# Performance work log

Measured on AMD Instinct MI355X. Metric: run time of the kernel, lower is better.

## Reference

```python
import jax, jax.numpy as jnp
import numpy as np
from jax import lax

K = 3          # kernel_size
PAD = 1        # replication padding
EPS = 1e-5     # BatchNorm2d eps


def setup_inputs() -> dict:
    key = jax.random.key(0)
    k1, k2, k3, k4 = jax.random.split(key, 4)
    B, Cin, O, H, W = 16, 64, 128, 32, 32
    x = jax.random.normal(k1, (B, Cin + 5, H, W), dtype=jnp.float32)
    conv_w = jax.random.normal(k2, (O, Cin, K, K), dtype=jnp.float32) * 0.05
    conv_b = jax.random.normal(k3, (O,), dtype=jnp.float32) * 0.05
    shapes_kernel = jax.random.normal(k4, (O, 5, K * K), dtype=jnp.float32)
    return {"x": x, "conv_w": conv_w, "conv_b": conv_b, "shapes_kernel": shapes_kernel}


def _bn_noaffine(y):
    # BatchNorm2d(affine=False) in training mode: batch stats over (N, H, W)
    m = jnp.mean(y, axis=(0, 2, 3), keepdims=True)
    v = jnp.mean((y - m) ** 2, axis=(0, 2, 3), keepdims=True)
    return (y - m) / jnp.sqrt(v + EPS)


def reference(x, conv_w, conv_b, shapes_kernel):
    B = x.shape[0]
    # replication padding
    xp = jnp.pad(x, ((0, 0), (0, 0), (PAD, PAD), (PAD, PAD)), mode="edge")
    feat, shp = xp[:, :-5], xp[:, -5:]

    # conv branch: VALID conv on feature channels -> (B, O, H, W)
    conv_out = lax.conv_general_dilated(
        feat, conv_w, window_strides=(1, 1), padding="VALID",
        dimension_numbers=("NCHW", "OIHW", "NCHW"),
    ) + conv_b[None, :, None, None]
    H, W = conv_out.shape[2], conv_out.shape[3]
    NW = H * W

    # unfold(x_padded[:, -5:], K): patches (B, 5, K*K, NW), channel-major like torch
    patches = jnp.stack(
        [shp[:, :, i:i + H, j:j + W] for i in range(K) for j in range(K)], axis=2
    ).reshape(B, 5, K * K, NW)

    # center the first two (x,y coordinate) channels on the window center
    c = K * K // 2
    centered_xy = patches[:, :2] - patches[:, :2, c:c + 1]
    windows = jnp.concatenate([centered_xy, patches[:, 2:]], axis=1)  # (B,5,KK,NW)

    # L1 distance against learned shape kernel: (B, O, NW)
    delta = windows[:, None] - shapes_kernel[None, :, :, :, None]  # (B,O,5,KK,NW)
    shape_difference = jnp.sum(jnp.abs(delta), axis=(2, 3))

    # fold with (1,1) kernel == reshape to image
    sdw = shape_difference.reshape(B, -1, H, W)
    muxed = jax.nn.relu(_bn_noaffine(sdw))

    conv_bn = _bn_noaffine(conv_out)
    attended = jax.nn.relu(conv_bn - muxed)

    # pass the 5 shape channels through unchanged
    return jnp.concatenate([attended, x[:, -5:]], axis=1)
```

## Files before the change

kernel.cpp:

```cpp
#include <hip/hip_runtime.h>

typedef __attribute__((ext_vector_type(8))) __bf16 bf16x8;
typedef __attribute__((ext_vector_type(4))) float f32x4;

#define NB 16
#define CIN 64
#define CT 69
#define NO 128
#define HWSZ 1024
#define OUTC 133

__device__ __forceinline__ unsigned pack_bf16(float a, float b) {
    unsigned ua = __float_as_uint(a);
    ua += 0x7fffu + ((ua >> 16) & 1u);
    unsigned ub = __float_as_uint(b);
    ub += 0x7fffu + ((ub >> 16) & 1u);
    return (ua >> 16) | (ub & 0xffff0000u);
}

__device__ __forceinline__ void gload16(const void* g, void* l) {
    __builtin_amdgcn_global_load_lds(
        (const __attribute__((address_space(1))) unsigned int*)g,
        (__attribute__((address_space(3))) unsigned int*)l, 16, 0, 0);
}

__global__ __launch_bounds__(512) void prep_sdw_kernel(
    const float* __restrict__ x, const float* __restrict__ cw,
    const float* __restrict__ sk, unsigned* __restrict__ xT,
    unsigned* __restrict__ wT, float* __restrict__ sdw,
    float* __restrict__ sdwpart, float* __restrict__ out)
{
    int bl = blockIdx.x;
    int tid = threadIdx.x;

    if (bl < 512) {
        int chg = bl >> 5;
        int slice = bl & 31;
        int pix = slice * 512 + tid;
        int b = pix >> 10;
        int hw = pix & 1023;
        int h = hw >> 5, w = hw & 31;

        float win[45];
#pragma unroll
        for (int ch = 0; ch < 5; ++ch) {
            const float* xb = x + (((size_t)b * CT + CIN + ch) << 10);
#pragma unroll
            for (int ki = 0; ki < 3; ++ki) {
                int rr = h + ki - 1;
                rr = rr < 0 ? 0 : (rr > 31 ? 31 : rr);
                const float* rp = xb + (rr << 5);
#pragma unroll
                for (int kj = 0; kj < 3; ++kj) {
                    int cc = w + kj - 1;
                    cc = cc < 0 ? 0 : (cc > 31 ? 31 : cc);
                    win[ch * 9 + ki * 3 + kj] = rp[cc];
                }
            }
        }
#pragma unroll
        for (int ch = 0; ch < 2; ++ch) {
            float c = win[ch * 9 + 4];
#pragma unroll
            for (int k = 0; k < 9; ++k) win[ch * 9 + k] -= c;
        }
#pragma unroll
        for (int q = 0; q < 45; ++q) asm volatile("" : "+v"(win[q]));

        int wid = tid >> 6;
        int wslot = slice * 8 + wid;
        for (int j = 0; j < 8; ++j) {
            int ch = chg * 8 + j;
            const float* kk = sk + (size_t)ch * 45;
            float s = 0.f;
#pragma unroll
            for (int q = 0; q < 45; ++q) s += fabsf(win[q] - kk[q]);
            sdw[(((size_t)b * NO + ch) << 10) + hw] = s;
            float ps = s, ps2 = s * s;
#pragma unroll
            for (int off = 32; off; off >>= 1) {
                ps  += __shfl_xor(ps, off);
                ps2 += __shfl_xor(ps2, off);
            }
            if ((tid & 63) == 0) {
                sdwpart[((size_t)ch * 256 + wslot) * 2]     = ps;
                sdwpart[((size_t)ch * 256 + wslot) * 2 + 1] = ps2;
            }
        }
    } else if (bl < 768) {
        int v = (bl - 512) * 512 + tid;
        int blk2 = v >> 8;
        int t2 = v & 255;
        int b = blk2 >> 5, h = blk2 & 31;
        int w = t2 & 31, cp0 = t2 >> 5;
        const float* xr = x + (((size_t)b * CT) << 10) + h * 32 + w;
        unsigned* dst = xT + (size_t)blk2 * 1024 + w * 32;
        int sw = (w & 7) << 2;
#pragma unroll
        for (int r = 0; r < 4; ++r) {
            int cp = cp0 + r * 8;
            dst[cp ^ sw] = pack_bf16(xr[(size_t)(2 * cp) << 10],
                                     xr[(size_t)(2 * cp + 1) << 10]);
        }
    } else if (bl < 776) {
        int tg = (bl - 768) * 512 + tid;
        int o = tg >> 5, cp = tg & 31;
        int sw = (o & 7) << 2;
#pragma unroll
        for (int tap = 0; tap < 9; ++tap) {
            float v0 = cw[((size_t)o * CIN + 2 * cp) * 9 + tap];
            float v1 = cw[((size_t)o * CIN + 2 * cp + 1) * 9 + tap];
            wT[tap * 4096 + o * 32 + (cp ^ sw)] = pack_bf16(v0, v1);
        }
    } else {
        int idx = (bl - 776) * 512 + tid;
        int q = idx & 255;
        int c = (idx >> 8) % 5;
        int b = (idx >> 8) / 5;
        ((float4*)out)[((size_t)b * OUTC + NO + c) * 256 + q] =
            ((const float4*)x)[((size_t)b * CT + CIN + c) * 256 + q];
    }
}

__global__ __launch_bounds__(512) void conv_mfma_kernel(
    const char* __restrict__ xT, const char* __restrict__ wT,
    float* __restrict__ out, float* __restrict__ convpart)
{
    __shared__ __align__(16) char smem[49152];
    char* Xs = smem;
    char* W0 = smem + 16384;
    char* W1 = smem + 32768;

    int bid = blockIdx.x;
    int b = bid >> 4;
    int h0 = (bid & 15) * 2;

    int tid = threadIdx.x;
    int lane = tid & 63;
    int wid = tid >> 6;
    int lo = lane & 15, g = lane >> 4;
    int ks = wid >> 2;
    int mg = (wid >> 1) & 1;
    int ng = wid & 1;

#pragma unroll
    for (int q = 0; q < 2; ++q) {
        int ch = wid * 2 + q;
        int s = ch >> 2;
        int srch = h0 - 1 + s; srch = srch < 0 ? 0 : (srch > 31 ? 31 : srch);
        gload16(xT + ((size_t)(b * 32 + srch)) * 4096 + (ch & 3) * 1024 + lane * 16,
                Xs + ch * 1024);
    }
#pragma unroll
    for (int q = 0; q < 2; ++q) {
        int ch = wid * 2 + q;
        gload16(wT + ch * 1024 + lane * 16, W0 + ch * 1024);
    }

    int acol[2][3];
#pragma unroll
    for (int i = 0; i < 2; ++i)
#pragma unroll
        for (int kj = 0; kj < 3; ++kj) {
            int cin = i * 16 + lo + kj - 1;
            cin = cin < 0 ? 0 : (cin > 31 ? 31 : cin);
            acol[i][kj] = cin * 128 + ((ks * 64 + g * 16) ^ ((cin & 7) << 4));
        }
    int boff[4];
#pragma unroll
    for (int n = 0; n < 4; ++n) {
        int o = ng * 64 + n * 16 + lo;
        boff[n] = o * 128 + ((ks * 64 + g * 16) ^ ((o & 7) << 4));
    }

    f32x4 acc[2][4];
#pragma unroll
    for (int i = 0; i < 2; ++i)
#pragma unroll
        for (int n = 0; n < 4; ++n) acc[i][n] = (f32x4){0.f, 0.f, 0.f, 0.f};

    __syncthreads();

#pragma unroll
    for (int tap = 0; tap < 9; ++tap) {
        int ki = tap / 3, kj = tap % 3;
        if (tap < 8) {
            char* wn = ((tap + 1) & 1) ? W1 : W0;
#pragma unroll
            for (int q = 0; q < 2; ++q) {
                int ch = wid * 2 + q;
                gload16(wT + (size_t)(tap + 1) * 16384 + ch * 1024 + lane * 16,
                        wn + ch * 1024);
            }
        }
        const char* wc = (tap & 1) ? W1 : W0;
        bf16x8 a0 = *(const bf16x8*)(Xs + (mg + ki) * 4096 + acol[0][kj]);
        bf16x8 a1 = *(const bf16x8*)(Xs + (mg + ki) * 4096 + acol[1][kj]);
#pragma unroll
        for (int n = 0; n < 4; ++n) {
            bf16x8 bv = *(const bf16x8*)(wc + boff[n]);
            acc[0][n] = __builtin_amdgcn_mfma_f32_16x16x32_bf16(a0, bv, acc[0][n], 0, 0, 0);
            acc[1][n] = __builtin_amdgcn_mfma_f32_16x16x32_bf16(a1, bv, acc[1][n], 0, 0, 0);
        }
        __syncthreads();
    }

    float* T = (float*)smem;
    if (ks == 1) {
#pragma unroll
        for (int i = 0; i < 2; ++i)
#pragma unroll
            for (int n = 0; n < 4; ++n)
#pragma unroll
                for (int r = 0; r < 4; ++r) {
                    int pixel = (mg * 2 + i) * 16 + g * 4 + r;
                    int o = ng * 64 + n * 16 + lo;
                    T[pixel * 129 + o] = acc[i][n][r];
                }
    }
    __syncthreads();
    if (ks == 0) {
#pragma unroll
        for (int i = 0; i < 2; ++i)
#pragma unroll
            for (int n = 0; n < 4; ++n)
#pragma unroll
                for (int r = 0; r < 4; ++r) {
                    int pixel = (mg * 2 + i) * 16 + g * 4 + r;
                    int o = ng * 64 + n * 16 + lo;
                    T[pixel * 129 + o] += acc[i][n][r];
                }
    }
    __syncthreads();
    float* obase = out + (((size_t)b * OUTC) << 10) + h0 * 32;
#pragma unroll
    for (int r = 0; r < 4; ++r) {
        int o = r * 32 + (tid >> 4);
        int pq = tid & 15;
        float4 v;
        v.x = T[(pq * 4 + 0) * 129 + o];
        v.y = T[(pq * 4 + 1) * 129 + o];
        v.z = T[(pq * 4 + 2) * 129 + o];
        v.w = T[(pq * 4 + 3) * 129 + o];
        *(float4*)(obase + ((size_t)o << 10) + pq * 4) = v;
        float s  = v.x + v.y + v.z + v.w;
        float s2 = v.x * v.x + v.y * v.y + v.z * v.z + v.w * v.w;
#pragma unroll
        for (int off = 1; off < 16; off <<= 1) {
            s  += __shfl_xor(s, off);
            s2 += __shfl_xor(s2, off);
        }
        if (pq == 0) {
            convpart[((size_t)o * 256 + bid) * 2]     = s;
            convpart[((size_t)o * 256 + bid) * 2 + 1] = s2;
        }
    }
}

__global__ __launch_bounds__(512) void final_kernel(
    const float* __restrict__ sdw, const float* __restrict__ convpart,
    const float* __restrict__ sdwpart, float* __restrict__ out)
{
    __shared__ float st[32];
    int bl = blockIdx.x;
    int tid = threadIdx.x;
    int b = bl >> 4;
    int o0 = (bl & 15) * 8;

    int lane = tid & 63;
    int wid = tid >> 6;
    {
        int ch = o0 + wid;
        double cs = 0.0, cs2 = 0.0, ss = 0.0, ss2 = 0.0;
#pragma unroll
        for (int q = 0; q < 4; ++q) {
            int slot = lane + q * 64;
            const float* cp = convpart + ((size_t)ch * 256 + slot) * 2;
            cs  += cp[0]; cs2 += cp[1];
            const float* sp = sdwpart + ((size_t)ch * 256 + slot) * 2;
            ss  += sp[0]; ss2 += sp[1];
        }
#pragma unroll
        for (int off = 32; off; off >>= 1) {
            cs  += __shfl_down(cs, off);
            cs2 += __shfl_down(cs2, off);
            ss  += __shfl_down(ss, off);
            ss2 += __shfl_down(ss2, off);
        }
        if (lane == 0) {
            double n = 16384.0;
            double cm = cs / n, cv = cs2 / n - cm * cm;
            double sm = ss / n, sv = ss2 / n - sm * sm;
            st[wid * 4]     = (float)cm;
            st[wid * 4 + 1] = (float)(1.0 / sqrt(cv + 1e-5));
            st[wid * 4 + 2] = (float)sm;
            st[wid * 4 + 3] = (float)(1.0 / sqrt(sv + 1e-5));
        }
    }
    __syncthreads();

    float4* outq = (float4*)out;
    const float4* sdwq = (const float4*)sdw;
#pragma unroll
    for (int k = 0; k < 4; ++k) {
        int ql = tid + k * 512;
        int pl = ql >> 8;
        int q = ql & 255;
        int o = o0 + pl;
        float4 cvv = outq[((size_t)b * OUTC + o) * 256 + q];
        float4 svv = sdwq[((size_t)b * NO + o) * 256 + q];
        float cm = st[pl * 4], cis = st[pl * 4 + 1];
        float sm = st[pl * 4 + 2], sis = st[pl * 4 + 3];
        float4 rv;
        {
            float mu = (svv.x - sm) * sis; mu = mu > 0.f ? mu : 0.f;
            float v = (cvv.x - cm) * cis - mu; rv.x = v > 0.f ? v : 0.f;
        }
        {
            float mu = (svv.y - sm) * sis; mu = mu > 0.f ? mu : 0.f;
            float v = (cvv.y - cm) * cis - mu; rv.y = v > 0.f ? v : 0.f;
        }
        {
            float mu = (svv.z - sm) * sis; mu = mu > 0.f ? mu : 0.f;
            float v = (cvv.z - cm) * cis - mu; rv.z = v > 0.f ? v : 0.f;
        }
        {
            float mu = (svv.w - sm) * sis; mu = mu > 0.f ? mu : 0.f;
            float v = (cvv.w - cm) * cis - mu; rv.w = v > 0.f ? v : 0.f;
        }
        outq[((size_t)b * OUTC + o) * 256 + q] = rv;
    }
}

extern "C" void kernel_launch(void* const* d_in, const int* in_sizes, int n_in,
                              void* d_out, int out_size, void* d_ws, size_t ws_size,
                              hipStream_t stream)
{
    const float* x  = (const float*)d_in[0];
    const float* cw = (const float*)d_in[1];
    const float* sk = (const float*)d_in[3];
    float* out = (float*)d_out;

    float*    sdw      = (float*)d_ws;
    unsigned* xT       = (unsigned*)((char*)d_ws + 0x810000);
    unsigned* wT       = (unsigned*)((char*)d_ws + 0xA10000);
    float*    convpart = (float*)((char*)d_ws + 0xA40000);
    float*    sdwpart  = (float*)((char*)d_ws + 0xA80000);

    prep_sdw_kernel<<<816, 512, 0, stream>>>(x, cw, sk, xT, wT, sdw, sdwpart, out);
    conv_mfma_kernel<<<256, 512, 0, stream>>>((const char*)xT, (const char*)wT,
                                              out, convpart);
    final_kernel   <<<256, 512, 0, stream>>>(sdw, convpart, sdwpart, out);
}
```

Baseline: 36.37 us.

## Fuse conv and final BN kernels via cooperative grid sync; triple-buffer weight loads

Merges the conv MFMA kernel and the final BN/ReLU kernel into one cooperative launch, using a grid-wide sync after the per-block statistics are written. This removes one kernel launch and its gap. It also switches the per-tap weight staging from double to triple buffering, with explicit vmcnt waits and one barrier per tap. The cost is a larger LDS footprint and the overhead of a cooperative launch plus a grid barrier. All 256 blocks must also be co-resident.

```diff
diff --git a/kernel.cpp b/kernel.cpp
--- a/kernel.cpp
+++ b/kernel.cpp
@@ -1,4 +1,7 @@
 #include <hip/hip_runtime.h>
+#include <hip/hip_cooperative_groups.h>
+
+namespace cg = cooperative_groups;
 
 typedef __attribute__((ext_vector_type(8))) __bf16 bf16x8;
 typedef __attribute__((ext_vector_type(4))) float f32x4;
@@ -122,14 +125,18 @@
     }
 }
 
-__global__ __launch_bounds__(512) void conv_mfma_kernel(
+__global__ __launch_bounds__(512) void conv_final_kernel(
     const char* __restrict__ xT, const char* __restrict__ wT,
-    float* __restrict__ out, float* __restrict__ convpart)
+    const float* __restrict__ sdw, float* __restrict__ convpart,
+    const float* __restrict__ sdwpart, float* __restrict__ out)
 {
-    __shared__ __align__(16) char smem[49152];
+    __shared__ __align__(16) char smem[65536];
+    cg::grid_group gg = cg::this_grid();
+
     char* Xs = smem;
-    char* W0 = smem + 16384;
-    char* W1 = smem + 32768;
+    char* Wb0 = smem + 16384;
+    char* Wb1 = smem + 32768;
+    char* Wb2 = smem + 49152;
 
     int bid = blockIdx.x;
     int b = bid >> 4;
@@ -154,7 +161,12 @@
 #pragma unroll
     for (int q = 0; q < 2; ++q) {
         int ch = wid * 2 + q;
-        gload16(wT + ch * 1024 + lane * 16, W0 + ch * 1024);
+        gload16(wT + ch * 1024 + lane * 16, Wb0 + ch * 1024);
+    }
+#pragma unroll
+    for (int q = 0; q < 2; ++q) {
+        int ch = wid * 2 + q;
+        gload16(wT + 16384 + ch * 1024 + lane * 16, Wb1 + ch * 1024);
     }
 
     int acol[2][3];
@@ -179,21 +191,24 @@
 #pragma unroll
         for (int n = 0; n < 4; ++n) acc[i][n] = (f32x4){0.f, 0.f, 0.f, 0.f};
 
-    __syncthreads();
-
 #pragma unroll
     for (int tap = 0; tap < 9; ++tap) {
         int ki = tap / 3, kj = tap % 3;
-        if (tap < 8) {
-            char* wn = ((tap + 1) & 1) ? W1 : W0;
+        if (tap == 8) asm volatile("s_waitcnt vmcnt(0)" ::: "memory");
+        else          asm volatile("s_waitcnt vmcnt(2)" ::: "memory");
+        __builtin_amdgcn_sched_barrier(0);
+        __builtin_amdgcn_s_barrier();
+        __builtin_amdgcn_sched_barrier(0);
+        if (tap + 2 < 9) {
+            char* wn = ((tap + 2) % 3 == 0) ? Wb0 : ((tap + 2) % 3 == 1) ? Wb1 : Wb2;
 #pragma unroll
             for (int q = 0; q < 2; ++q) {
                 int ch = wid * 2 + q;
-                gload16(wT + (size_t)(tap + 1) * 16384 + ch * 1024 + lane * 16,
+                gload16(wT + (size_t)(tap + 2) * 16384 + ch * 1024 + lane * 16,
                         wn + ch * 1024);
             }
         }
-        const char* wc = (tap & 1) ? W1 : W0;
+        const char* wc = (tap % 3 == 0) ? Wb0 : (tap % 3 == 1) ? Wb1 : Wb2;
         bf16x8 a0 = *(const bf16x8*)(Xs + (mg + ki) * 4096 + acol[0][kj]);
         bf16x8 a1 = *(const bf16x8*)(Xs + (mg + ki) * 4096 + acol[1][kj]);
 #pragma unroll
@@ -202,8 +217,8 @@
             acc[0][n] = __builtin_amdgcn_mfma_f32_16x16x32_bf16(a0, bv, acc[0][n], 0, 0, 0);
             acc[1][n] = __builtin_amdgcn_mfma_f32_16x16x32_bf16(a1, bv, acc[1][n], 0, 0, 0);
         }
-        __syncthreads();
-    }
+    }
+    __syncthreads();
 
     float* T = (float*)smem;
     if (ks == 1) {
@@ -255,80 +270,74 @@
             convpart[((size_t)o * 256 + bid) * 2 + 1] = s2;
         }
     }
-}
-
-__global__ __launch_bounds__(512) void final_kernel(
-    const float* __restrict__ sdw, const float* __restrict__ convpart,
-    const float* __restrict__ sdwpart, float* __restrict__ out)
-{
-    __shared__ float st[32];
-    int bl = blockIdx.x;
-    int tid = threadIdx.x;
-    int b = bl >> 4;
-    int o0 = (bl & 15) * 8;
-
-    int lane = tid & 63;
-    int wid = tid >> 6;
+
+    __threadfence();
+    gg.sync();
+
     {
-        int ch = o0 + wid;
-        double cs = 0.0, cs2 = 0.0, ss = 0.0, ss2 = 0.0;
-#pragma unroll
-        for (int q = 0; q < 4; ++q) {
-            int slot = lane + q * 64;
-            const float* cp = convpart + ((size_t)ch * 256 + slot) * 2;
-            cs  += cp[0]; cs2 += cp[1];
-            const float* sp = sdwpart + ((size_t)ch * 256 + slot) * 2;
-            ss  += sp[0]; ss2 += sp[1];
-        }
-#pragma unroll
-        for (int off = 32; off; off >>= 1) {
-            cs  += __shfl_down(cs, off);
-            cs2 += __shfl_down(cs2, off);
-            ss  += __shfl_down(ss, off);
-            ss2 += __shfl_down(ss2, off);
-        }
-        if (lane == 0) {
-            double n = 16384.0;
-            double cm = cs / n, cv = cs2 / n - cm * cm;
-            double sm = ss / n, sv = ss2 / n - sm * sm;
-            st[wid * 4]     = (float)cm;
-            st[wid * 4 + 1] = (float)(1.0 / sqrt(cv + 1e-5));
-            st[wid * 4 + 2] = (float)sm;
-            st[wid * 4 + 3] = (float)(1.0 / sqrt(sv + 1e-5));
-        }
-    }
-    __syncthreads();
-
-    float4* outq = (float4*)out;
-    const float4* sdwq = (const float4*)sdw;
-#pragma unroll
-    for (int k = 0; k < 4; ++k) {
-        int ql = tid + k * 512;
-        int pl = ql >> 8;
-        int q = ql & 255;
-        int o = o0 + pl;
-        float4 cvv = outq[((size_t)b * OUTC + o) * 256 + q];
-        float4 svv = sdwq[((size_t)b * NO + o) * 256 + q];
-        float cm = st[pl * 4], cis = st[pl * 4 + 1];
-        float sm = st[pl * 4 + 2], sis = st[pl * 4 + 3];
-        float4 rv;
+        float* st = (float*)smem;
+        int o0 = (bid & 15) * 8;
         {
-            float mu = (svv.x - sm) * sis; mu = mu > 0.f ? mu : 0.f;
-            float v = (cvv.x - cm) * cis - mu; rv.x = v > 0.f ? v : 0.f;
-        }
-        {
-            float mu = (svv.y - sm) * sis; mu = mu > 0.f ? mu : 0.f;
-            float v = (cvv.y - cm) * cis - mu; rv.y = v > 0.f ? v : 0.f;
-        }
-        {
-            float mu = (svv.z - sm) * sis; mu = mu > 0.f ? mu : 0.f;
-            float v = (cvv.z - cm) * cis - mu; rv.z = v > 0.f ? v : 0.f;
-        }
-        {
-            float mu = (svv.w - sm) * sis; mu = mu > 0.f ? mu : 0.f;
-            float v = (cvv.w - cm) * cis - mu; rv.w = v > 0.f ? v : 0.f;
-        }
-        outq[((size_t)b * OUTC + o) * 256 + q] = rv;
+            int ch = o0 + wid;
+            double cs = 0.0, cs2 = 0.0, ss = 0.0, ss2 = 0.0;
+#pragma unroll
+            for (int q = 0; q < 4; ++q) {
+                int slot = lane + q * 64;
+                const float* cp = convpart + ((size_t)ch * 256 + slot) * 2;
+                cs  += cp[0]; cs2 += cp[1];
+                const float* sp = sdwpart + ((size_t)ch * 256 + slot) * 2;
+                ss  += sp[0]; ss2 += sp[1];
+            }
+#pragma unroll
+            for (int off = 32; off; off >>= 1) {
+                cs  += __shfl_down(cs, off);
+                cs2 += __shfl_down(cs2, off);
+                ss  += __shfl_down(ss, off);
+                ss2 += __shfl_down(ss2, off);
+            }
+            if (lane == 0) {
+                double n = 16384.0;
+                double cm = cs / n, cv = cs2 / n - cm * cm;
+                double sm = ss / n, sv = ss2 / n - sm * sm;
+                st[wid * 4]     = (float)cm;
+                st[wid * 4 + 1] = (float)(1.0 / sqrt(cv + 1e-5));
+                st[wid * 4 + 2] = (float)sm;
+                st[wid * 4 + 3] = (float)(1.0 / sqrt(sv + 1e-5));
+            }
+        }
+        __syncthreads();
+
+        float4* outq = (float4*)out;
+        const float4* sdwq = (const float4*)sdw;
+#pragma unroll
+        for (int k = 0; k < 4; ++k) {
+            int ql = tid + k * 512;
+            int pl = ql >> 8;
+            int q = ql & 255;
+            int o = o0 + pl;
+            float4 cvv = outq[((size_t)b * OUTC + o) * 256 + q];
+            float4 svv = sdwq[((size_t)b * NO + o) * 256 + q];
+            float cm = st[pl * 4], cis = st[pl * 4 + 1];
+            float sm = st[pl * 4 + 2], sis = st[pl * 4 + 3];
+            float4 rv;
+            {
+                float mu = (svv.x - sm) * sis; mu = mu > 0.f ? mu : 0.f;
+                float v = (cvv.x - cm) * cis - mu; rv.x = v > 0.f ? v : 0.f;
+            }
+            {
+                float mu = (svv.y - sm) * sis; mu = mu > 0.f ? mu : 0.f;
+                float v = (cvv.y - cm) * cis - mu; rv.y = v > 0.f ? v : 0.f;
+            }
+            {
+                float mu = (svv.z - sm) * sis; mu = mu > 0.f ? mu : 0.f;
+                float v = (cvv.z - cm) * cis - mu; rv.z = v > 0.f ? v : 0.f;
+            }
+            {
+                float mu = (svv.w - sm) * sis; mu = mu > 0.f ? mu : 0.f;
+                float v = (cvv.w - cm) * cis - mu; rv.w = v > 0.f ? v : 0.f;
+            }
+            outq[((size_t)b * OUTC + o) * 256 + q] = rv;
+        }
     }
 }
 
@@ -348,7 +357,13 @@
     float*    sdwpart  = (float*)((char*)d_ws + 0xA80000);
 
     prep_sdw_kernel<<<816, 512, 0, stream>>>(x, cw, sk, xT, wT, sdw, sdwpart, out);
-    conv_mfma_kernel<<<256, 512, 0, stream>>>((const char*)xT, (const char*)wT,
-                                              out, convpart);
-    final_kernel   <<<256, 512, 0, stream>>>(sdw, convpart, sdwpart, out);
-}
+
+    const char* xTc = (const char*)xT;
+    const char* wTc = (const char*)wT;
+    const float* sdwc = sdw;
+    const float* sdwpartc = sdwpart;
+    void* args[] = {(void*)&xTc, (void*)&wTc, (void*)&sdwc,
+                    (void*)&convpart, (void*)&sdwpartc, (void*)&out};
+    hipLaunchCooperativeKernel((const void*)conv_final_kernel, dim3(256), dim3(512),
+                               args, 0, stream);
+}
```

Measured after the change: 121.0 us. +232.8%, slower.

## Fuse final BN kernel into conv kernel via software grid barrier

Applied to the files above, without the earlier changes.

Merges the final normalization/ReLU kernel into the conv MFMA kernel, separated by an atomic-counter grid-wide barrier that is reset in the prep kernel. This removes one kernel launch and the gap between launches. It relies on all 256 blocks being co-resident on the GPU, which holds on a large part but would deadlock otherwise. The epilogue reuses the conv kernel's LDS for the per-channel stats.

```diff
diff --git a/kernel.cpp b/kernel.cpp
--- a/kernel.cpp
+++ b/kernel.cpp
@@ -28,7 +28,8 @@
     const float* __restrict__ x, const float* __restrict__ cw,
     const float* __restrict__ sk, unsigned* __restrict__ xT,
     unsigned* __restrict__ wT, float* __restrict__ sdw,
-    float* __restrict__ sdwpart, float* __restrict__ out)
+    float* __restrict__ sdwpart, float* __restrict__ out,
+    unsigned* __restrict__ barflag)
 {
     int bl = blockIdx.x;
     int tid = threadIdx.x;
@@ -119,12 +120,17 @@
         int b = (idx >> 8) / 5;
         ((float4*)out)[((size_t)b * OUTC + NO + c) * 256 + q] =
             ((const float4*)x)[((size_t)b * CT + CIN + c) * 256 + q];
-    }
-}
-
-__global__ __launch_bounds__(512) void conv_mfma_kernel(
+        if (bl == 815 && tid == 0)
+            __hip_atomic_store(barflag, 0u, __ATOMIC_RELAXED,
+                               __HIP_MEMORY_SCOPE_AGENT);
+    }
+}
+
+__global__ __launch_bounds__(512) void conv_final_kernel(
     const char* __restrict__ xT, const char* __restrict__ wT,
-    float* __restrict__ out, float* __restrict__ convpart)
+    const float* __restrict__ sdw, float* __restrict__ convpart,
+    const float* __restrict__ sdwpart, float* __restrict__ out,
+    unsigned* __restrict__ barflag)
 {
     __shared__ __align__(16) char smem[49152];
     char* Xs = smem;
@@ -255,80 +261,84 @@
             convpart[((size_t)o * 256 + bid) * 2 + 1] = s2;
         }
     }
-}
-
-__global__ __launch_bounds__(512) void final_kernel(
-    const float* __restrict__ sdw, const float* __restrict__ convpart,
-    const float* __restrict__ sdwpart, float* __restrict__ out)
-{
-    __shared__ float st[32];
-    int bl = blockIdx.x;
-    int tid = threadIdx.x;
-    int b = bl >> 4;
-    int o0 = (bl & 15) * 8;
-
-    int lane = tid & 63;
-    int wid = tid >> 6;
+
+    __threadfence();
+    __syncthreads();
+    if (tid == 0) {
+        __hip_atomic_fetch_add(barflag, 1u, __ATOMIC_ACQ_REL,
+                               __HIP_MEMORY_SCOPE_AGENT);
+        while (__hip_atomic_load(barflag, __ATOMIC_ACQUIRE,
+                                 __HIP_MEMORY_SCOPE_AGENT) < 256u) {
+            __builtin_amdgcn_s_sleep(8);
+        }
+    }
+    __syncthreads();
+    __threadfence();
+
     {
-        int ch = o0 + wid;
-        double cs = 0.0, cs2 = 0.0, ss = 0.0, ss2 = 0.0;
-#pragma unroll
-        for (int q = 0; q < 4; ++q) {
-            int slot = lane + q * 64;
-            const float* cp = convpart + ((size_t)ch * 256 + slot) * 2;
-            cs  += cp[0]; cs2 += cp[1];
-            const float* sp = sdwpart + ((size_t)ch * 256 + slot) * 2;
-            ss  += sp[0]; ss2 += sp[1];
-        }
-#pragma unroll
-        for (int off = 32; off; off >>= 1) {
-            cs  += __shfl_down(cs, off);
-            cs2 += __shfl_down(cs2, off);
-            ss  += __shfl_down(ss, off);
-            ss2 += __shfl_down(ss2, off);
-        }
-        if (lane == 0) {
-            double n = 16384.0;
-            double cm = cs / n, cv = cs2 / n - cm * cm;
-            double sm = ss / n, sv = ss2 / n - sm * sm;
-            st[wid * 4]     = (float)cm;
-            st[wid * 4 + 1] = (float)(1.0 / sqrt(cv + 1e-5));
-            st[wid * 4 + 2] = (float)sm;
-            st[wid * 4 + 3] = (float)(1.0 / sqrt(sv + 1e-5));
-        }
-    }
-    __syncthreads();
-
-    float4* outq = (float4*)out;
-    const float4* sdwq = (const float4*)sdw;
-#pragma unroll
-    for (int k = 0; k < 4; ++k) {
-        int ql = tid + k * 512;
-        int pl = ql >> 8;
-        int q = ql & 255;
-        int o = o0 + pl;
-        float4 cvv = outq[((size_t)b * OUTC + o) * 256 + q];
-        float4 svv = sdwq[((size_t)b * NO + o) * 256 + q];
-        float cm = st[pl * 4], cis = st[pl * 4 + 1];
-        float sm = st[pl * 4 + 2], sis = st[pl * 4 + 3];
-        float4 rv;
+        float* st = (float*)smem;
+        int o0 = (bid & 15) * 8;
         {
-            float mu = (svv.x - sm) * sis; mu = mu > 0.f ? mu : 0.f;
-            float v = (cvv.x - cm) * cis - mu; rv.x = v > 0.f ? v : 0.f;
-        }
-        {
-            float mu = (svv.y - sm) * sis; mu = mu > 0.f ? mu : 0.f;
-            float v = (cvv.y - cm) * cis - mu; rv.y = v > 0.f ? v : 0.f;
-        }
-        {
-            float mu = (svv.z - sm) * sis; mu = mu > 0.f ? mu : 0.f;
-            float v = (cvv.z - cm) * cis - mu; rv.z = v > 0.f ? v : 0.f;
-        }
-        {
-            float mu = (svv.w - sm) * sis; mu = mu > 0.f ? mu : 0.f;
-            float v = (cvv.w - cm) * cis - mu; rv.w = v > 0.f ? v : 0.f;
-        }
-        outq[((size_t)b * OUTC + o) * 256 + q] = rv;
+            int ch = o0 + wid;
+            double cs = 0.0, cs2 = 0.0, ss = 0.0, ss2 = 0.0;
+#pragma unroll
+            for (int q = 0; q < 4; ++q) {
+                int slot = lane + q * 64;
+                const float* cp = convpart + ((size_t)ch * 256 + slot) * 2;
+                cs  += cp[0]; cs2 += cp[1];
+                const float* sp = sdwpart + ((size_t)ch * 256 + slot) * 2;
+                ss  += sp[0]; ss2 += sp[1];
+            }
+#pragma unroll
+            for (int off = 32; off; off >>= 1) {
+                cs  += __shfl_down(cs, off);
+                cs2 += __shfl_down(cs2, off);
+                ss  += __shfl_down(ss, off);
+                ss2 += __shfl_down(ss2, off);
+            }
+            if (lane == 0) {
+                double n = 16384.0;
+                double cm = cs / n, cv = cs2 / n - cm * cm;
+                double sm = ss / n, sv = ss2 / n - sm * sm;
+                st[wid * 4]     = (float)cm;
+                st[wid * 4 + 1] = (float)(1.0 / sqrt(cv + 1e-5));
+                st[wid * 4 + 2] = (float)sm;
+                st[wid * 4 + 3] = (float)(1.0 / sqrt(sv + 1e-5));
+            }
+        }
+        __syncthreads();
+
+        float4* outq = (float4*)out;
+        const float4* sdwq = (const float4*)sdw;
+#pragma unroll
+        for (int k = 0; k < 4; ++k) {
+            int ql = tid + k * 512;
+            int pl = ql >> 8;
+            int q = ql & 255;
+            int o = o0 + pl;
+            float4 cvv = outq[((size_t)b * OUTC + o) * 256 + q];
+            float4 svv = sdwq[((size_t)b * NO + o) * 256 + q];
+            float cm = st[pl * 4], cis = st[pl * 4 + 1];
+            float sm = st[pl * 4 + 2], sis = st[pl * 4 + 3];
+            float4 rv;
+            {
+                float mu = (svv.x - sm) * sis; mu = mu > 0.f ? mu : 0.f;
+                float v = (cvv.x - cm) * cis - mu; rv.x = v > 0.f ? v : 0.f;
+            }
+            {
+                float mu = (svv.y - sm) * sis; mu = mu > 0.f ? mu : 0.f;
+                float v = (cvv.y - cm) * cis - mu; rv.y = v > 0.f ? v : 0.f;
+            }
+            {
+                float mu = (svv.z - sm) * sis; mu = mu > 0.f ? mu : 0.f;
+                float v = (cvv.z - cm) * cis - mu; rv.z = v > 0.f ? v : 0.f;
+            }
+            {
+                float mu = (svv.w - sm) * sis; mu = mu > 0.f ? mu : 0.f;
+                float v = (cvv.w - cm) * cis - mu; rv.w = v > 0.f ? v : 0.f;
+            }
+            outq[((size_t)b * OUTC + o) * 256 + q] = rv;
+        }
     }
 }
 
@@ -346,9 +356,10 @@
     unsigned* wT       = (unsigned*)((char*)d_ws + 0xA10000);
     float*    convpart = (float*)((char*)d_ws + 0xA40000);
     float*    sdwpart  = (float*)((char*)d_ws + 0xA80000);
-
-    prep_sdw_kernel<<<816, 512, 0, stream>>>(x, cw, sk, xT, wT, sdw, sdwpart, out);
-    conv_mfma_kernel<<<256, 512, 0, stream>>>((const char*)xT, (const char*)wT,
-                                              out, convpart);
-    final_kernel   <<<256, 512, 0, stream>>>(sdw, convpart, sdwpart, out);
-}
+    unsigned* barflag  = (unsigned*)((char*)d_ws + 0xAC0000);
+
+    prep_sdw_kernel<<<816, 512, 0, stream>>>(x, cw, sk, xT, wT, sdw, sdwpart,
+                                             out, barflag);
+    conv_final_kernel<<<256, 512, 0, stream>>>((const char*)xT, (const char*)wT,
+                                               sdw, convpart, sdwpart, out, barflag);
+}
```

New measurement: 116.2 us. 219% more time.
